# Kernel optimization log

Measured on AMD Instinct MI355X. Metric: run time of the kernel, lower is better.

The kernel has to match this reference:

```python
import jax, jax.numpy as jnp
import numpy as np

V, E, H, B, S, T = 32000, 256, 256, 64, 512, 256


def setup_inputs() -> dict:
    key = jax.random.key(0)
    ks = jax.random.split(key, 24)
    def w(i, shape, scale=0.05):
        return jax.random.normal(ks[i], shape, jnp.float32) * scale
    return {
        "pre_seq": jax.random.randint(ks[0], (B, S), 0, V),
        "post_seq": jax.random.randint(ks[1], (B, S), 0, V),
        "trg": jax.random.randint(ks[2], (B, T), 0, V),
        "emb": w(3, (V, E)),
        "Wi_pre": w(4, (3 * H, E)), "Wh_pre": w(5, (3 * H, H)),
        "bi_pre": w(6, (3 * H,)), "bh_pre": w(7, (3 * H,)),
        "Wi_post": w(8, (3 * H, E)), "Wh_post": w(9, (3 * H, H)),
        "bi_post": w(10, (3 * H,)), "bh_post": w(11, (3 * H,)),
        "Wfc": w(12, (H, 2 * H)), "bfc": w(13, (H,)),
        "Wi_dec": w(14, (3 * H, E)), "Wh_dec": w(15, (3 * H, H)),
        "bi_dec": w(16, (3 * H,)), "bh_dec": w(17, (3 * H,)),
        "w_hid": w(18, (1, 2 * H)), "b_hid": w(19, (1,)),
        "w_out": w(20, (1, 1)), "b_out": w(21, (1,)),
    }


def gru_cell(h, x, Wi, Wh, bi, bh):
    # torch nn.GRU gating convention, gates ordered (r, z, n)
    gi = x @ Wi.T + bi              # (B, 3H)
    gh = h @ Wh.T + bh              # (B, 3H)
    ir, iz, inn = jnp.split(gi, 3, axis=-1)
    hr, hz, hn = jnp.split(gh, 3, axis=-1)
    r = jax.nn.sigmoid(ir + hr)
    z = jax.nn.sigmoid(iz + hz)
    n = jnp.tanh(inn + r * hn)
    return (1.0 - z) * n + z * h


def gru_seq(seq_emb, Wi, Wh, bi, bh):
    # seq_emb: (B, L, E) -> outputs (B, L, H), final hidden (B, H)
    h0 = jnp.zeros((seq_emb.shape[0], Wh.shape[1]), seq_emb.dtype)
    def step(h, x):
        h = gru_cell(h, x, Wi, Wh, bi, bh)
        return h, h
    hT, outs = jax.lax.scan(step, h0, jnp.swapaxes(seq_emb, 0, 1))
    return jnp.swapaxes(outs, 0, 1), hT


def reference(pre_seq, post_seq, trg, emb, Wi_pre, Wh_pre, bi_pre, bh_pre,
              Wi_post, Wh_post, bi_post, bh_post, Wfc, bfc,
              Wi_dec, Wh_dec, bi_dec, bh_dec, w_hid, b_hid, w_out, b_out):
    # Encoder: two GRUs over pre/post token embeddings (dropout off / eval mode)
    pre_out, pre_h = gru_seq(emb[pre_seq], Wi_pre, Wh_pre, bi_pre, bh_pre)
    post_out, post_h = gru_seq(emb[post_seq], Wi_post, Wh_post, bi_post, bh_post)
    enc_out = jnp.concatenate([pre_out, post_out], axis=1)          # (B, 2S, H)
    h0 = jnp.tanh(jnp.concatenate([pre_h, post_h], axis=-1) @ Wfc.T + bfc)  # (B, H)

    # fc_hid(relu(cat([enc_out, h_t]))) splits into a step-constant enc term
    # and a per-step hidden term since relu acts elementwise on the concat.
    A = jax.nn.relu(enc_out) @ w_hid[0, :H]                         # (B, 2S)

    # Teacher-forced decoder inputs: last pre token, then trg[:, :-1]
    in_toks = jnp.concatenate([pre_seq[:, -1:], trg[:, :-1]], axis=1)  # (B, T)

    def step(h, tok):
        x = emb[tok]                                                # (B, E)
        h = gru_cell(h, x, Wi_dec, Wh_dec, bi_dec, bh_dec)          # (B, H)
        s = jax.nn.relu(h) @ w_hid[0, H:]                           # (B,)
        out = (A + s[:, None] + b_hid[0]) * w_out[0, 0] + b_out[0]  # (B, 2S)
        return h, out

    _, outs = jax.lax.scan(step, h0, in_toks.T)                     # (T, B, 2S)
    outs = jnp.swapaxes(outs, 0, 1)                                 # (B, T, 2S)
    return outs[:, :, :S], outs[:, :, S:]
```

## Files before the change

### kernel.cpp

```cpp
#include <hip/hip_runtime.h>
#include <stdint.h>

typedef _Float16 f16;
typedef _Float16 half2_t __attribute__((ext_vector_type(2)));
typedef _Float16 half8_t __attribute__((ext_vector_type(8)));
typedef float    f32x4_t __attribute__((ext_vector_type(4)));
typedef uint32_t u32x32  __attribute__((ext_vector_type(32)));

constexpr int NB = 64, NS = 512, NT = 256, NE = 256, NH = 256;
constexpr int G3 = 768;

static __device__ __forceinline__ float sigm(float x){ return 1.f/(1.f+__expf(-x)); }
static __device__ __forceinline__ float tanhfast(float x){
  float e = __expf(-2.f*x);
  return (1.f-e)/(1.f+e);
}
static __device__ __forceinline__ uint32_t pack2(float a, float b){
  half2_t h; h[0]=(f16)a; h[1]=(f16)b;
  return __builtin_bit_cast(uint32_t, h);
}
static __device__ __forceinline__ float dot2f(uint32_t w, uint32_t h, float acc){
#if __has_builtin(__builtin_amdgcn_fdot2)
  return __builtin_amdgcn_fdot2(__builtin_bit_cast(half2_t,w),
                                __builtin_bit_cast(half2_t,h), acc, false);
#else
  half2_t a = __builtin_bit_cast(half2_t,w), b = __builtin_bit_cast(half2_t,h);
  return acc + (float)a[0]*(float)b[0] + (float)a[1]*(float)b[1];
#endif
}
static __device__ __forceinline__ half8_t cvt8(float4 a, float4 b){
  half8_t p;
  p[0]=(f16)a.x; p[1]=(f16)a.y; p[2]=(f16)a.z; p[3]=(f16)a.w;
  p[4]=(f16)b.x; p[5]=(f16)b.y; p[6]=(f16)b.z; p[7]=(f16)b.w;
  return p;
}

#define LOAD_W(WSRC)                                                         \
  _Pragma("unroll")                                                          \
  for (int i=0;i<32;++i){                                                    \
    wr0[i]=(WSRC)[(size_t)i*G3];          wr1[i]=(WSRC)[(size_t)(i+32)*G3];  \
    wz0[i]=(WSRC)[(size_t)i*G3+256];      wz1[i]=(WSRC)[(size_t)(i+32)*G3+256];\
    wn0[i]=(WSRC)[(size_t)i*G3+512];      wn1[i]=(WSRC)[(size_t)(i+32)*G3+512];\
  }

#define DOT_BLOCK(W_R, W_Z, W_N, HPTR)                                       \
  _Pragma("unroll")                                                          \
  for (int c=0;c<4;++c){                                                     \
    uint4 ha = *(const uint4*)((HPTR) + c*8);                                \
    uint4 hb = *(const uint4*)((HPTR) + c*8 + 4);                            \
    uint32_t hh0=ha.x,hh1=ha.y,hh2=ha.z,hh3=ha.w;                            \
    uint32_t hh4=hb.x,hh5=hb.y,hh6=hb.z,hh7=hb.w;                            \
    a0=dot2f(W_R[c*8+0],hh0,a0); a1=dot2f(W_Z[c*8+0],hh0,a1); a2=dot2f(W_N[c*8+0],hh0,a2); \
    a0=dot2f(W_R[c*8+1],hh1,a0); a1=dot2f(W_Z[c*8+1],hh1,a1); a2=dot2f(W_N[c*8+1],hh1,a2); \
    a0=dot2f(W_R[c*8+2],hh2,a0); a1=dot2f(W_Z[c*8+2],hh2,a1); a2=dot2f(W_N[c*8+2],hh2,a2); \
    a0=dot2f(W_R[c*8+3],hh3,a0); a1=dot2f(W_Z[c*8+3],hh3,a1); a2=dot2f(W_N[c*8+3],hh3,a2); \
    a0=dot2f(W_R[c*8+4],hh4,a0); a1=dot2f(W_Z[c*8+4],hh4,a1); a2=dot2f(W_N[c*8+4],hh4,a2); \
    a0=dot2f(W_R[c*8+5],hh5,a0); a1=dot2f(W_Z[c*8+5],hh5,a1); a2=dot2f(W_N[c*8+5],hh5,a2); \
    a0=dot2f(W_R[c*8+6],hh6,a0); a1=dot2f(W_Z[c*8+6],hh6,a1); a2=dot2f(W_N[c*8+6],hh6,a2); \
    a0=dot2f(W_R[c*8+7],hh7,a0); a1=dot2f(W_Z[c*8+7],hh7,a1); a2=dot2f(W_N[c*8+7],hh7,a2); \
  }

__global__ __launch_bounds__(256) void k_prep(const float* __restrict__ Wh_pre,
                                              const float* __restrict__ Wh_post,
                                              const float* __restrict__ Wh_dec,
                                              uint32_t* __restrict__ WhT_pre,
                                              uint32_t* __restrict__ WhT_post,
                                              uint32_t* __restrict__ WhT_dec,
                                              const int* __restrict__ pre_seq,
                                              const int* __restrict__ trg,
                                              int* __restrict__ in_toks){
  int bid = blockIdx.x;
  if (bid < 1152){
    const float* Wh = (bid < 384) ? Wh_pre : (bid < 768) ? Wh_post : Wh_dec;
    uint32_t* out   = (bid < 384) ? WhT_pre : (bid < 768) ? WhT_post : WhT_dec;
    int idx = (bid % 384)*256 + threadIdx.x;
    int kp = idx / G3, row = idx % G3;
    out[idx] = pack2(Wh[(size_t)row*NE + 2*kp], Wh[(size_t)row*NE + 2*kp + 1]);
  } else {
    int idx = (bid - 1152)*256 + threadIdx.x;
    int b = idx >> 8, t = idx & 255;
    in_toks[idx] = (t == 0) ? pre_seq[b*NS + NS-1] : trg[b*NT + t - 1];
  }
}

__global__ __launch_bounds__(256) void k_gemm_gi(const float* __restrict__ emb,
                                                 const int* __restrict__ toks,
                                                 const float* __restrict__ Wi,
                                                 const float* __restrict__ bi,
                                                 f16* __restrict__ out){
  __shared__ f16 As[128][72];
  __shared__ f16 Bs[128][72];
  const int tid = threadIdx.x;
  const int m0 = blockIdx.x*128, n0 = blockIdx.y*128;
  const int lane = tid & 63, wid = tid >> 6;
  const int wm = wid >> 1, wn = wid & 1;
  const int fr = lane & 15, fq = lane >> 4;

  f32x4_t acc[4][4];
  #pragma unroll
  for (int i=0;i<4;++i)
    #pragma unroll
    for (int j=0;j<4;++j){ acc[i][j][0]=0.f; acc[i][j][1]=0.f; acc[i][j][2]=0.f; acc[i][j][3]=0.f; }

  const int r = tid >> 1, hh = tid & 1;
  const int tok = toks[m0 + r];
  const float* asrc = emb + (size_t)tok*NE + hh*32;
  const float* bsrc = Wi  + (size_t)(n0 + r)*NE + hh*32;

  for (int k0 = 0; k0 < NE; k0 += 64){
    #pragma unroll
    for (int c=0;c<4;++c){
      float4 x0 = *(const float4*)(asrc + k0 + c*8);
      float4 x1 = *(const float4*)(asrc + k0 + c*8 + 4);
      *(half8_t*)&As[r][hh*32 + c*8] = cvt8(x0, x1);
      float4 y0 = *(const float4*)(bsrc + k0 + c*8);
      float4 y1 = *(const float4*)(bsrc + k0 + c*8 + 4);
      *(half8_t*)&Bs[r][hh*32 + c*8] = cvt8(y0, y1);
    }
    __syncthreads();
    #pragma unroll
    for (int kk=0; kk<2; ++kk){
      half8_t af[4], bf[4];
      #pragma unroll
      for (int m=0;m<4;++m) af[m] = *(const half8_t*)&As[wm*64 + m*16 + fr][kk*32 + fq*8];
      #pragma unroll
      for (int n=0;n<4;++n) bf[n] = *(const half8_t*)&Bs[wn*64 + n*16 + fr][kk*32 + fq*8];
      #pragma unroll
      for (int m=0;m<4;++m)
        #pragma unroll
        for (int n=0;n<4;++n)
          acc[m][n] = __builtin_amdgcn_mfma_f32_16x16x32_f16(af[m], bf[n], acc[m][n], 0,0,0);
    }
    __syncthreads();
  }
  #pragma unroll
  for (int n=0;n<4;++n){
    const int col = n0 + wn*64 + n*16 + fr;
    const float bv = bi[col];
    #pragma unroll
    for (int m=0;m<4;++m){
      const int rowb = m0 + wm*64 + m*16 + fq*4;
      #pragma unroll
      for (int j=0;j<4;++j)
        out[(size_t)(rowb + j)*G3 + col] = (f16)(acc[m][n][j] + bv);
    }
  }
}

__global__ __launch_bounds__(512, 2) void k_enc(const uint32_t* __restrict__ WhT_pre,
                                                const uint32_t* __restrict__ WhT_post,
                                                const f16* __restrict__ gi_pre,
                                                const f16* __restrict__ gi_post,
                                                const float* __restrict__ bh_pre,
                                                const float* __restrict__ bh_post,
                                                const float* __restrict__ w_hid,
                                                float* __restrict__ Abuf,
                                                float* __restrict__ preh,
                                                float* __restrict__ posth){
  __shared__ __align__(16) uint32_t h_pair[128];
  __shared__ float part[3][256];
  __shared__ float ared[4];

  const int b = blockIdx.x & 63, which = blockIdx.x >> 6;
  const int tid = threadIdx.x;
  const int n = tid & 255, half = tid >> 8;

  const uint32_t* WhT = which ? WhT_post : WhT_pre;
  const f16* gi = (which ? gi_post : gi_pre) + (size_t)b*NS*G3;
  const float* bh = which ? bh_post : bh_pre;

  u32x32 wr0, wr1, wz0, wz1, wn0, wn1;
  {
    const uint32_t* wsrc = WhT + (size_t)(half*64)*G3 + n;
    LOAD_W(wsrc);
  }
  const float bh0 = bh[n], bh1 = bh[256+n], bh2 = bh[512+n];
  const float whv = w_hid[n];
  float hreg = 0.f;
  if (tid < 128) h_pair[tid] = 0u;
  __syncthreads();

  float* Arow = Abuf + b*1024 + which*512;

  for (int t=0; t<NS; ++t){
    float g0=0.f, g1=0.f, g2=0.f;
    if (half == 0){
      const f16* gp = gi + (size_t)t*G3;
      g0 = (float)gp[n]; g1 = (float)gp[256+n]; g2 = (float)gp[512+n];
    }
    float a0=0.f, a1=0.f, a2=0.f;
    const uint32_t* hp = h_pair + half*64;
    DOT_BLOCK(wr0, wz0, wn0, hp);
    DOT_BLOCK(wr1, wz1, wn1, hp + 32);
    if (half == 1){ part[0][n]=a0; part[1][n]=a1; part[2][n]=a2; }
    __syncthreads();
    if (half == 0){
      float ghr = a0 + part[0][n] + bh0;
      float ghz = a1 + part[1][n] + bh1;
      float ghn = a2 + part[2][n] + bh2;
      float rg = sigm(g0 + ghr);
      float zg = sigm(g1 + ghz);
      float nn = tanhfast(g2 + rg*ghn);
      float hnew = (1.f - zg)*nn + zg*hreg;
      hreg = hnew;
      float hnb = __shfl_down(hnew, 1);
      if ((n & 1) == 0) h_pair[n >> 1] = pack2(hnew, hnb);
      float redv = fmaxf(hnew, 0.f) * whv;
      #pragma unroll
      for (int off=32; off; off>>=1) redv += __shfl_down(redv, off);
      if ((tid & 63) == 0) ared[tid >> 6] = redv;
    }
    __syncthreads();
    if (tid == 0) Arow[t] = ared[0]+ared[1]+ared[2]+ared[3];
  }
  if (half == 0) (which ? posth : preh)[b*NH + n] = hreg;
}

__global__ __launch_bounds__(512, 2) void k_dec(const uint32_t* __restrict__ WhT,
                                                const f16* __restrict__ gi,
                                                const float* __restrict__ bh,
                                                const float* __restrict__ w_hid,
                                                const float* __restrict__ Wfc,
                                                const float* __restrict__ bfc,
                                                const float* __restrict__ preh,
                                                const float* __restrict__ posth,
                                                float* __restrict__ sbuf){
  __shared__ __align__(16) uint32_t h_pair[128];
  __shared__ float part[3][256];
  __shared__ float ared[4];
  __shared__ float hcat[512];

  const int b = blockIdx.x;
  const int tid = threadIdx.x;
  const int n = tid & 255, half = tid >> 8;

  const float bh0 = bh[n], bh1 = bh[256+n], bh2 = bh[512+n];
  const float whv = w_hid[NH + n];
  float hreg = 0.f;

  hcat[tid] = (tid < 256) ? preh[b*NH + tid] : posth[b*NH + tid - 256];
  __syncthreads();
  {
    const float* wrow = Wfc + (size_t)n*512 + half*256;
    const float* hc = hcat + half*256;
    float acc = 0.f;
    #pragma unroll 4
    for (int j=0;j<256;j+=4){
      float4 wv = *(const float4*)(wrow + j);
      acc = fmaf(wv.x, hc[j],   acc);
      acc = fmaf(wv.y, hc[j+1], acc);
      acc = fmaf(wv.z, hc[j+2], acc);
      acc = fmaf(wv.w, hc[j+3], acc);
    }
    if (half == 1) part[0][n] = acc;
    __syncthreads();
    if (half == 0){
      float h0 = tanhfast(acc + part[0][n] + bfc[n]);
      hreg = h0;
      float hnb = __shfl_down(h0, 1);
      if ((n & 1) == 0) h_pair[n >> 1] = pack2(h0, hnb);
    }
    __syncthreads();
  }

  u32x32 wr0, wr1, wz0, wz1, wn0, wn1;
  {
    const uint32_t* wsrc = WhT + (size_t)(half*64)*G3 + n;
    LOAD_W(wsrc);
  }

  const f16* gib = gi + (size_t)b*NT*G3;
  for (int t=0; t<NT; ++t){
    float g0=0.f, g1=0.f, g2=0.f;
    if (half == 0){
      const f16* gp = gib + (size_t)t*G3;
      g0 = (float)gp[n]; g1 = (float)gp[256+n]; g2 = (float)gp[512+n];
    }
    float a0=0.f, a1=0.f, a2=0.f;
    const uint32_t* hp = h_pair + half*64;
    DOT_BLOCK(wr0, wz0, wn0, hp);
    DOT_BLOCK(wr1, wz1, wn1, hp + 32);
    if (half == 1){ part[0][n]=a0; part[1][n]=a1; part[2][n]=a2; }
    __syncthreads();
    if (half == 0){
      float ghr = a0 + part[0][n] + bh0;
      float ghz = a1 + part[1][n] + bh1;
      float ghn = a2 + part[2][n] + bh2;
      float rg = sigm(g0 + ghr);
      float zg = sigm(g1 + ghz);
      float nn = tanhfast(g2 + rg*ghn);
      float hnew = (1.f - zg)*nn + zg*hreg;
      hreg = hnew;
      float hnb = __shfl_down(hnew, 1);
      if ((n & 1) == 0) h_pair[n >> 1] = pack2(hnew, hnb);
      float redv = fmaxf(hnew, 0.f) * whv;
      #pragma unroll
      for (int off=32; off; off>>=1) redv += __shfl_down(redv, off);
      if ((tid & 63) == 0) ared[tid >> 6] = redv;
    }
    __syncthreads();
    if (tid == 0) sbuf[b*NT + t] = ared[0]+ared[1]+ared[2]+ared[3];
  }
}

__global__ __launch_bounds__(256) void k_final(const float* __restrict__ Abuf,
                                               const float* __restrict__ sbuf,
                                               const float* __restrict__ b_hid,
                                               const float* __restrict__ w_out,
                                               const float* __restrict__ b_out,
                                               float* __restrict__ out){
  const float bh = b_hid[0], wo = w_out[0], bo = b_out[0];
  const int idx = blockIdx.x*256 + threadIdx.x;
  const int j4 = idx & 127, t = (idx >> 7) & 255, b = idx >> 15;
  const float sv = sbuf[b*NT + t] + bh;
  const float4 a0 = *(const float4*)(Abuf + b*1024 + j4*4);
  const float4 a1 = *(const float4*)(Abuf + b*1024 + 512 + j4*4);
  float4 o0, o1;
  o0.x = (a0.x + sv)*wo + bo; o0.y = (a0.y + sv)*wo + bo;
  o0.z = (a0.z + sv)*wo + bo; o0.w = (a0.w + sv)*wo + bo;
  o1.x = (a1.x + sv)*wo + bo; o1.y = (a1.y + sv)*wo + bo;
  o1.z = (a1.z + sv)*wo + bo; o1.w = (a1.w + sv)*wo + bo;
  float4* o = (float4*)out;
  o[idx] = o0;
  o[(size_t)(NB*NT*NS/4) + idx] = o1;
}

extern "C" void kernel_launch(void* const* d_in, const int* in_sizes, int n_in,
                              void* d_out, int out_size, void* d_ws, size_t ws_size,
                              hipStream_t stream){
  const int*   pre_seq = (const int*)d_in[0];
  const int*   post_seq= (const int*)d_in[1];
  const int*   trg     = (const int*)d_in[2];
  const float* emb     = (const float*)d_in[3];
  const float* Wi_pre  = (const float*)d_in[4];
  const float* Wh_pre  = (const float*)d_in[5];
  const float* bi_pre  = (const float*)d_in[6];
  const float* bh_pre  = (const float*)d_in[7];
  const float* Wi_post = (const float*)d_in[8];
  const float* Wh_post = (const float*)d_in[9];
  const float* bi_post = (const float*)d_in[10];
  const float* bh_post = (const float*)d_in[11];
  const float* Wfc     = (const float*)d_in[12];
  const float* bfc     = (const float*)d_in[13];
  const float* Wi_dec  = (const float*)d_in[14];
  const float* Wh_dec  = (const float*)d_in[15];
  const float* bi_dec  = (const float*)d_in[16];
  const float* bh_dec  = (const float*)d_in[17];
  const float* w_hid   = (const float*)d_in[18];
  const float* b_hid   = (const float*)d_in[19];
  const float* w_out   = (const float*)d_in[20];
  const float* b_out   = (const float*)d_in[21];

  char* wp = (char*)d_ws;
  f16* gi_pre  = (f16*)wp; wp += (size_t)NB*NS*G3*2;
  f16* gi_post = (f16*)wp; wp += (size_t)NB*NS*G3*2;
  f16* gi_dec  = (f16*)wp; wp += (size_t)NB*NT*G3*2;
  uint32_t* WhT_pre  = (uint32_t*)wp; wp += (size_t)128*G3*4;
  uint32_t* WhT_post = (uint32_t*)wp; wp += (size_t)128*G3*4;
  uint32_t* WhT_dec  = (uint32_t*)wp; wp += (size_t)128*G3*4;
  int*   in_toks = (int*)wp;   wp += (size_t)NB*NT*4;
  float* Abuf    = (float*)wp; wp += (size_t)NB*1024*4;
  float* sbuf    = (float*)wp; wp += (size_t)NB*NT*4;
  float* preh    = (float*)wp; wp += (size_t)NB*NH*4;
  float* posth   = (float*)wp; wp += (size_t)NB*NH*4;
  (void)ws_size; (void)in_sizes; (void)n_in; (void)out_size;

  k_prep<<<1216, 256, 0, stream>>>(Wh_pre, Wh_post, Wh_dec,
                                   WhT_pre, WhT_post, WhT_dec,
                                   pre_seq, trg, in_toks);

  k_gemm_gi<<<dim3(256,6), 256, 0, stream>>>(emb, pre_seq,  Wi_pre,  bi_pre,  gi_pre);
  k_gemm_gi<<<dim3(256,6), 256, 0, stream>>>(emb, post_seq, Wi_post, bi_post, gi_post);
  k_gemm_gi<<<dim3(128,6), 256, 0, stream>>>(emb, in_toks,  Wi_dec,  bi_dec,  gi_dec);

  k_enc<<<128, 512, 0, stream>>>(WhT_pre, WhT_post, gi_pre, gi_post,
                                 bh_pre, bh_post, w_hid, Abuf, preh, posth);
  k_dec<<<64, 512, 0, stream>>>(WhT_dec, gi_dec, bh_dec, w_hid, Wfc, bfc,
                                preh, posth, sbuf);
  k_final<<<NB*NT*NS/4/256, 256, 0, stream>>>(Abuf, sbuf, b_hid, w_out, b_out,
                                              (float*)d_out);
}
```

Before: 1.280 ms.

## Split GRU recurrent matvec across four thread quarters with redundant gate math

The encoder and decoder recurrent kernels move from 512 to 1024 threads per block, so each thread holds a quarter of the K dimension (96 weight registers instead of 192) pinned with asm barriers. All four quarters exchange partial sums through shared memory and compute the gate nonlinearities redundantly, so no thread sits idle after the barrier. The hidden state is now stored as plain f16 rather than packed pairs via shuffle. The reduction result for each step is written lazily at the start of the next step, which drops one barrier per step. The aim is to shorten the per-step serial critical path. The cost is more shared-memory traffic and 1024-thread blocks with one block per CU.

Result: slower. 1.417 ms (+10.7%).

```diff
diff --git a/kernel.cpp b/kernel.cpp
--- a/kernel.cpp
+++ b/kernel.cpp
@@ -5,7 +5,7 @@
 typedef _Float16 half2_t __attribute__((ext_vector_type(2)));
 typedef _Float16 half8_t __attribute__((ext_vector_type(8)));
 typedef float    f32x4_t __attribute__((ext_vector_type(4)));
-typedef uint32_t u32x32  __attribute__((ext_vector_type(32)));
+typedef uint32_t u32x4   __attribute__((ext_vector_type(4)));
 
 constexpr int NB = 64, NS = 512, NT = 256, NE = 256, NH = 256;
 constexpr int G3 = 768;
@@ -35,30 +35,29 @@
   return p;
 }
 
-#define LOAD_W(WSRC)                                                         \
-  _Pragma("unroll")                                                          \
-  for (int i=0;i<32;++i){                                                    \
-    wr0[i]=(WSRC)[(size_t)i*G3];          wr1[i]=(WSRC)[(size_t)(i+32)*G3];  \
-    wz0[i]=(WSRC)[(size_t)i*G3+256];      wz1[i]=(WSRC)[(size_t)(i+32)*G3+256];\
-    wn0[i]=(WSRC)[(size_t)i*G3+512];      wn1[i]=(WSRC)[(size_t)(i+32)*G3+512];\
-  }
-
-#define DOT_BLOCK(W_R, W_Z, W_N, HPTR)                                       \
-  _Pragma("unroll")                                                          \
-  for (int c=0;c<4;++c){                                                     \
-    uint4 ha = *(const uint4*)((HPTR) + c*8);                                \
-    uint4 hb = *(const uint4*)((HPTR) + c*8 + 4);                            \
-    uint32_t hh0=ha.x,hh1=ha.y,hh2=ha.z,hh3=ha.w;                            \
-    uint32_t hh4=hb.x,hh5=hb.y,hh6=hb.z,hh7=hb.w;                            \
-    a0=dot2f(W_R[c*8+0],hh0,a0); a1=dot2f(W_Z[c*8+0],hh0,a1); a2=dot2f(W_N[c*8+0],hh0,a2); \
-    a0=dot2f(W_R[c*8+1],hh1,a0); a1=dot2f(W_Z[c*8+1],hh1,a1); a2=dot2f(W_N[c*8+1],hh1,a2); \
-    a0=dot2f(W_R[c*8+2],hh2,a0); a1=dot2f(W_Z[c*8+2],hh2,a1); a2=dot2f(W_N[c*8+2],hh2,a2); \
-    a0=dot2f(W_R[c*8+3],hh3,a0); a1=dot2f(W_Z[c*8+3],hh3,a1); a2=dot2f(W_N[c*8+3],hh3,a2); \
-    a0=dot2f(W_R[c*8+4],hh4,a0); a1=dot2f(W_Z[c*8+4],hh4,a1); a2=dot2f(W_N[c*8+4],hh4,a2); \
-    a0=dot2f(W_R[c*8+5],hh5,a0); a1=dot2f(W_Z[c*8+5],hh5,a1); a2=dot2f(W_N[c*8+5],hh5,a2); \
-    a0=dot2f(W_R[c*8+6],hh6,a0); a1=dot2f(W_Z[c*8+6],hh6,a1); a2=dot2f(W_N[c*8+6],hh6,a2); \
-    a0=dot2f(W_R[c*8+7],hh7,a0); a1=dot2f(W_Z[c*8+7],hh7,a1); a2=dot2f(W_N[c*8+7],hh7,a2); \
-  }
+#define DECLW(P, GO, C)                                                      \
+  uint32_t P##C##_0 = wsrc[(size_t)((C)*4+0)*G3 + (GO)];                     \
+  uint32_t P##C##_1 = wsrc[(size_t)((C)*4+1)*G3 + (GO)];                     \
+  uint32_t P##C##_2 = wsrc[(size_t)((C)*4+2)*G3 + (GO)];                     \
+  uint32_t P##C##_3 = wsrc[(size_t)((C)*4+3)*G3 + (GO)];                     \
+  asm volatile("" : "+v"(P##C##_0), "+v"(P##C##_1), "+v"(P##C##_2), "+v"(P##C##_3));
+
+#define DECL_ALL_W \
+  DECLW(wa,0,0) DECLW(wa,0,1) DECLW(wa,0,2) DECLW(wa,0,3)                    \
+  DECLW(wa,0,4) DECLW(wa,0,5) DECLW(wa,0,6) DECLW(wa,0,7)                    \
+  DECLW(wb,256,0) DECLW(wb,256,1) DECLW(wb,256,2) DECLW(wb,256,3)            \
+  DECLW(wb,256,4) DECLW(wb,256,5) DECLW(wb,256,6) DECLW(wb,256,7)            \
+  DECLW(wc,512,0) DECLW(wc,512,1) DECLW(wc,512,2) DECLW(wc,512,3)            \
+  DECLW(wc,512,4) DECLW(wc,512,5) DECLW(wc,512,6) DECLW(wc,512,7)
+
+#define DOTC(C) {                                                            \
+    u32x4 hq = *(const u32x4*)(h32q + 4*(C));                                \
+    a0=dot2f(wa##C##_0,hq[0],a0); a1=dot2f(wb##C##_0,hq[0],a1); a2=dot2f(wc##C##_0,hq[0],a2); \
+    a0=dot2f(wa##C##_1,hq[1],a0); a1=dot2f(wb##C##_1,hq[1],a1); a2=dot2f(wc##C##_1,hq[1],a2); \
+    a0=dot2f(wa##C##_2,hq[2],a0); a1=dot2f(wb##C##_2,hq[2],a1); a2=dot2f(wc##C##_2,hq[2],a2); \
+    a0=dot2f(wa##C##_3,hq[3],a0); a1=dot2f(wb##C##_3,hq[3],a1); a2=dot2f(wc##C##_3,hq[3],a2); }
+
+#define DOT_ALL DOTC(0) DOTC(1) DOTC(2) DOTC(3) DOTC(4) DOTC(5) DOTC(6) DOTC(7)
 
 __global__ __launch_bounds__(256) void k_prep(const float* __restrict__ Wh_pre,
                                               const float* __restrict__ Wh_post,
@@ -147,160 +146,162 @@
   }
 }
 
-__global__ __launch_bounds__(512, 2) void k_enc(const uint32_t* __restrict__ WhT_pre,
-                                                const uint32_t* __restrict__ WhT_post,
-                                                const f16* __restrict__ gi_pre,
-                                                const f16* __restrict__ gi_post,
-                                                const float* __restrict__ bh_pre,
-                                                const float* __restrict__ bh_post,
-                                                const float* __restrict__ w_hid,
-                                                float* __restrict__ Abuf,
-                                                float* __restrict__ preh,
-                                                float* __restrict__ posth){
-  __shared__ __align__(16) uint32_t h_pair[128];
-  __shared__ float part[3][256];
+__global__ __launch_bounds__(1024) void k_enc(const uint32_t* __restrict__ WhT_pre,
+                                              const uint32_t* __restrict__ WhT_post,
+                                              const f16* __restrict__ gi_pre,
+                                              const f16* __restrict__ gi_post,
+                                              const float* __restrict__ bh_pre,
+                                              const float* __restrict__ bh_post,
+                                              const float* __restrict__ w_hid,
+                                              float* __restrict__ Abuf,
+                                              float* __restrict__ preh,
+                                              float* __restrict__ posth){
+  __shared__ __align__(16) f16 hh16[256];
+  __shared__ __align__(16) float part[4][256][4];
   __shared__ float ared[4];
 
   const int b = blockIdx.x & 63, which = blockIdx.x >> 6;
   const int tid = threadIdx.x;
-  const int n = tid & 255, half = tid >> 8;
+  const int n = tid & 255, q = tid >> 8;
 
   const uint32_t* WhT = which ? WhT_post : WhT_pre;
-  const f16* gi = (which ? gi_post : gi_pre) + (size_t)b*NS*G3;
   const float* bh = which ? bh_post : bh_pre;
 
-  u32x32 wr0, wr1, wz0, wz1, wn0, wn1;
-  {
-    const uint32_t* wsrc = WhT + (size_t)(half*64)*G3 + n;
-    LOAD_W(wsrc);
-  }
+  const uint32_t* wsrc = WhT + (size_t)(q*32)*G3 + n;
+  DECL_ALL_W
+
   const float bh0 = bh[n], bh1 = bh[256+n], bh2 = bh[512+n];
   const float whv = w_hid[n];
   float hreg = 0.f;
-  if (tid < 128) h_pair[tid] = 0u;
+  if (tid < 128) ((uint32_t*)hh16)[tid] = 0u;
   __syncthreads();
 
   float* Arow = Abuf + b*1024 + which*512;
-
+  const uint32_t* h32q = (const uint32_t*)hh16 + q*32;
+  const f16* gp = (which ? gi_post : gi_pre) + (size_t)b*NS*G3 + n;
+
+  #pragma unroll 1
   for (int t=0; t<NS; ++t){
-    float g0=0.f, g1=0.f, g2=0.f;
-    if (half == 0){
-      const f16* gp = gi + (size_t)t*G3;
-      g0 = (float)gp[n]; g1 = (float)gp[256+n]; g2 = (float)gp[512+n];
-    }
+    if (tid == 768 && t > 0) Arow[t-1] = ared[0]+ared[1]+ared[2]+ared[3];
+    f16 gr16 = gp[0], gz16 = gp[256], gn16 = gp[512];
+    gp += G3;
     float a0=0.f, a1=0.f, a2=0.f;
-    const uint32_t* hp = h_pair + half*64;
-    DOT_BLOCK(wr0, wz0, wn0, hp);
-    DOT_BLOCK(wr1, wz1, wn1, hp + 32);
-    if (half == 1){ part[0][n]=a0; part[1][n]=a1; part[2][n]=a2; }
-    __syncthreads();
-    if (half == 0){
-      float ghr = a0 + part[0][n] + bh0;
-      float ghz = a1 + part[1][n] + bh1;
-      float ghn = a2 + part[2][n] + bh2;
-      float rg = sigm(g0 + ghr);
-      float zg = sigm(g1 + ghz);
-      float nn = tanhfast(g2 + rg*ghn);
-      float hnew = (1.f - zg)*nn + zg*hreg;
-      hreg = hnew;
-      float hnb = __shfl_down(hnew, 1);
-      if ((n & 1) == 0) h_pair[n >> 1] = pack2(hnew, hnb);
+    DOT_ALL
+    *(f32x4_t*)&part[q][n][0] = (f32x4_t){a0, a1, a2, 0.f};
+    __syncthreads();
+    float s0=a0, s1=a1, s2=a2;
+    {
+      f32x4_t p1 = *(const f32x4_t*)&part[(q+1)&3][n][0];
+      s0+=p1[0]; s1+=p1[1]; s2+=p1[2];
+      f32x4_t p2 = *(const f32x4_t*)&part[(q+2)&3][n][0];
+      s0+=p2[0]; s1+=p2[1]; s2+=p2[2];
+      f32x4_t p3 = *(const f32x4_t*)&part[(q+3)&3][n][0];
+      s0+=p3[0]; s1+=p3[1]; s2+=p3[2];
+    }
+    float rg = sigm((float)gr16 + s0 + bh0);
+    float zg = sigm((float)gz16 + s1 + bh1);
+    float nn = tanhfast((float)gn16 + rg*(s2 + bh2));
+    float hnew = (1.f - zg)*nn + zg*hreg;
+    hreg = hnew;
+    if (q == 0) hh16[n] = (f16)hnew;
+    if (q == 1){
       float redv = fmaxf(hnew, 0.f) * whv;
       #pragma unroll
       for (int off=32; off; off>>=1) redv += __shfl_down(redv, off);
-      if ((tid & 63) == 0) ared[tid >> 6] = redv;
-    }
-    __syncthreads();
-    if (tid == 0) Arow[t] = ared[0]+ared[1]+ared[2]+ared[3];
-  }
-  if (half == 0) (which ? posth : preh)[b*NH + n] = hreg;
-}
-
-__global__ __launch_bounds__(512, 2) void k_dec(const uint32_t* __restrict__ WhT,
-                                                const f16* __restrict__ gi,
-                                                const float* __restrict__ bh,
-                                                const float* __restrict__ w_hid,
-                                                const float* __restrict__ Wfc,
-                                                const float* __restrict__ bfc,
-                                                const float* __restrict__ preh,
-                                                const float* __restrict__ posth,
-                                                float* __restrict__ sbuf){
-  __shared__ __align__(16) uint32_t h_pair[128];
-  __shared__ float part[3][256];
+      if ((tid & 63) == 0) ared[(tid >> 6) & 3] = redv;
+    }
+    __syncthreads();
+  }
+  if (tid == 768) Arow[NS-1] = ared[0]+ared[1]+ared[2]+ared[3];
+  if (q == 0) (which ? posth : preh)[b*NH + n] = hreg;
+}
+
+__global__ __launch_bounds__(1024) void k_dec(const uint32_t* __restrict__ WhT,
+                                              const f16* __restrict__ gi,
+                                              const float* __restrict__ bh,
+                                              const float* __restrict__ w_hid,
+                                              const float* __restrict__ Wfc,
+                                              const float* __restrict__ bfc,
+                                              const float* __restrict__ preh,
+                                              const float* __restrict__ posth,
+                                              float* __restrict__ sbuf){
+  __shared__ __align__(16) f16 hh16[256];
+  __shared__ __align__(16) float part[4][256][4];
   __shared__ float ared[4];
   __shared__ float hcat[512];
 
   const int b = blockIdx.x;
   const int tid = threadIdx.x;
-  const int n = tid & 255, half = tid >> 8;
+  const int n = tid & 255, q = tid >> 8;
+
+  const uint32_t* wsrc = WhT + (size_t)(q*32)*G3 + n;
+  DECL_ALL_W
 
   const float bh0 = bh[n], bh1 = bh[256+n], bh2 = bh[512+n];
   const float whv = w_hid[NH + n];
-  float hreg = 0.f;
-
-  hcat[tid] = (tid < 256) ? preh[b*NH + tid] : posth[b*NH + tid - 256];
+  float hreg;
+
+  if (tid < 256) hcat[tid] = preh[b*NH + tid];
+  else if (tid < 512) hcat[tid] = posth[b*NH + tid - 256];
   __syncthreads();
   {
-    const float* wrow = Wfc + (size_t)n*512 + half*256;
-    const float* hc = hcat + half*256;
+    const float* wrow = Wfc + (size_t)n*512 + q*128;
+    const float* hc = hcat + q*128;
     float acc = 0.f;
     #pragma unroll 4
-    for (int j=0;j<256;j+=4){
+    for (int j=0;j<128;j+=4){
       float4 wv = *(const float4*)(wrow + j);
       acc = fmaf(wv.x, hc[j],   acc);
       acc = fmaf(wv.y, hc[j+1], acc);
       acc = fmaf(wv.z, hc[j+2], acc);
       acc = fmaf(wv.w, hc[j+3], acc);
     }
-    if (half == 1) part[0][n] = acc;
-    __syncthreads();
-    if (half == 0){
-      float h0 = tanhfast(acc + part[0][n] + bfc[n]);
-      hreg = h0;
-      float hnb = __shfl_down(h0, 1);
-      if ((n & 1) == 0) h_pair[n >> 1] = pack2(h0, hnb);
-    }
-    __syncthreads();
-  }
-
-  u32x32 wr0, wr1, wz0, wz1, wn0, wn1;
-  {
-    const uint32_t* wsrc = WhT + (size_t)(half*64)*G3 + n;
-    LOAD_W(wsrc);
-  }
-
-  const f16* gib = gi + (size_t)b*NT*G3;
+    part[q][n][0] = acc;
+    __syncthreads();
+    float s = part[0][n][0] + part[1][n][0] + part[2][n][0] + part[3][n][0];
+    float h0 = tanhfast(s + bfc[n]);
+    hreg = h0;
+    if (q == 0) hh16[n] = (f16)h0;
+    __syncthreads();
+  }
+
+  float* srow = sbuf + b*NT;
+  const uint32_t* h32q = (const uint32_t*)hh16 + q*32;
+  const f16* gp = gi + (size_t)b*NT*G3 + n;
+
+  #pragma unroll 1
   for (int t=0; t<NT; ++t){
-    float g0=0.f, g1=0.f, g2=0.f;
-    if (half == 0){
-      const f16* gp = gib + (size_t)t*G3;
-      g0 = (float)gp[n]; g1 = (float)gp[256+n]; g2 = (float)gp[512+n];
-    }
+    if (tid == 768 && t > 0) srow[t-1] = ared[0]+ared[1]+ared[2]+ared[3];
+    f16 gr16 = gp[0], gz16 = gp[256], gn16 = gp[512];
+    gp += G3;
     float a0=0.f, a1=0.f, a2=0.f;
-    const uint32_t* hp = h_pair + half*64;
-    DOT_BLOCK(wr0, wz0, wn0, hp);
-    DOT_BLOCK(wr1, wz1, wn1, hp + 32);
-    if (half == 1){ part[0][n]=a0; part[1][n]=a1; part[2][n]=a2; }
-    __syncthreads();
-    if (half == 0){
-      float ghr = a0 + part[0][n] + bh0;
-      float ghz = a1 + part[1][n] + bh1;
-      float ghn = a2 + part[2][n] + bh2;
-      float rg = sigm(g0 + ghr);
-      float zg = sigm(g1 + ghz);
-      float nn = tanhfast(g2 + rg*ghn);
-      float hnew = (1.f - zg)*nn + zg*hreg;
-      hreg = hnew;
-      float hnb = __shfl_down(hnew, 1);
-      if ((n & 1) == 0) h_pair[n >> 1] = pack2(hnew, hnb);
+    DOT_ALL
+    *(f32x4_t*)&part[q][n][0] = (f32x4_t){a0, a1, a2, 0.f};
+    __syncthreads();
+    float s0=a0, s1=a1, s2=a2;
+    {
+      f32x4_t p1 = *(const f32x4_t*)&part[(q+1)&3][n][0];
+      s0+=p1[0]; s1+=p1[1]; s2+=p1[2];
+      f32x4_t p2 = *(const f32x4_t*)&part[(q+2)&3][n][0];
+      s0+=p2[0]; s1+=p2[1]; s2+=p2[2];
+      f32x4_t p3 = *(const f32x4_t*)&part[(q+3)&3][n][0];
+      s0+=p3[0]; s1+=p3[1]; s2+=p3[2];
+    }
+    float rg = sigm((float)gr16 + s0 + bh0);
+    float zg = sigm((float)gz16 + s1 + bh1);
+    float nn = tanhfast((float)gn16 + rg*(s2 + bh2));
+    float hnew = (1.f - zg)*nn + zg*hreg;
+    hreg = hnew;
+    if (q == 0) hh16[n] = (f16)hnew;
+    if (q == 1){
       float redv = fmaxf(hnew, 0.f) * whv;
       #pragma unroll
       for (int off=32; off; off>>=1) redv += __shfl_down(redv, off);
-      if ((tid & 63) == 0) ared[tid >> 6] = redv;
-    }
-    __syncthreads();
-    if (tid == 0) sbuf[b*NT + t] = ared[0]+ared[1]+ared[2]+ared[3];
-  }
+      if ((tid & 63) == 0) ared[(tid >> 6) & 3] = redv;
+    }
+    __syncthreads();
+  }
+  if (tid == 768) srow[NT-1] = ared[0]+ared[1]+ared[2]+ared[3];
 }
 
 __global__ __launch_bounds__(256) void k_final(const float* __restrict__ Abuf,
@@ -373,10 +374,10 @@
   k_gemm_gi<<<dim3(256,6), 256, 0, stream>>>(emb, post_seq, Wi_post, bi_post, gi_post);
   k_gemm_gi<<<dim3(128,6), 256, 0, stream>>>(emb, in_toks,  Wi_dec,  bi_dec,  gi_dec);
 
-  k_enc<<<128, 512, 0, stream>>>(WhT_pre, WhT_post, gi_pre, gi_post,
-                                 bh_pre, bh_post, w_hid, Abuf, preh, posth);
-  k_dec<<<64, 512, 0, stream>>>(WhT_dec, gi_dec, bh_dec, w_hid, Wfc, bfc,
-                                preh, posth, sbuf);
+  k_enc<<<128, 1024, 0, stream>>>(WhT_pre, WhT_post, gi_pre, gi_post,
+                                  bh_pre, bh_post, w_hid, Abuf, preh, posth);
+  k_dec<<<64, 1024, 0, stream>>>(WhT_dec, gi_dec, bh_dec, w_hid, Wfc, bfc,
+                                 preh, posth, sbuf);
   k_final<<<NB*NT*NS/4/256, 256, 0, stream>>>(Abuf, sbuf, b_hid, w_out, b_out,
                                               (float*)d_out);
 }
```

## Split recurrent weights between registers and per-step streamed global loads

Applied to the files above, without the earlier changes.

Each thread now keeps only half of its recurrent weight slice in registers (the first 32 k-pairs per gate) and streams the other half from a newly prepacked, coalesced global layout every timestep with inline global_load_dwordx4 and manual vmcnt waits. The loads are interleaved with the register-resident dot products so memory latency overlaps compute. The goal is to cut register pressure, which was holding 192 weight registers per thread, possibly to avoid spills or allow better scheduling. The cost is repeated L2 traffic for the weights on every step of a latency-bound serial recurrence, plus a larger prep kernel.

Measured after the change: 1.973 ms. +54.2%, slower.

```diff
diff --git a/kernel.cpp b/kernel.cpp
--- a/kernel.cpp
+++ b/kernel.cpp
@@ -5,7 +5,7 @@
 typedef _Float16 half2_t __attribute__((ext_vector_type(2)));
 typedef _Float16 half8_t __attribute__((ext_vector_type(8)));
 typedef float    f32x4_t __attribute__((ext_vector_type(4)));
-typedef uint32_t u32x32  __attribute__((ext_vector_type(32)));
+typedef uint32_t u32x4   __attribute__((ext_vector_type(4)));
 
 constexpr int NB = 64, NS = 512, NT = 256, NE = 256, NH = 256;
 constexpr int G3 = 768;
@@ -35,30 +35,61 @@
   return p;
 }
 
-#define LOAD_W(WSRC)                                                         \
-  _Pragma("unroll")                                                          \
-  for (int i=0;i<32;++i){                                                    \
-    wr0[i]=(WSRC)[(size_t)i*G3];          wr1[i]=(WSRC)[(size_t)(i+32)*G3];  \
-    wz0[i]=(WSRC)[(size_t)i*G3+256];      wz1[i]=(WSRC)[(size_t)(i+32)*G3+256];\
-    wn0[i]=(WSRC)[(size_t)i*G3+512];      wn1[i]=(WSRC)[(size_t)(i+32)*G3+512];\
-  }
-
-#define DOT_BLOCK(W_R, W_Z, W_N, HPTR)                                       \
-  _Pragma("unroll")                                                          \
-  for (int c=0;c<4;++c){                                                     \
-    uint4 ha = *(const uint4*)((HPTR) + c*8);                                \
-    uint4 hb = *(const uint4*)((HPTR) + c*8 + 4);                            \
-    uint32_t hh0=ha.x,hh1=ha.y,hh2=ha.z,hh3=ha.w;                            \
-    uint32_t hh4=hb.x,hh5=hb.y,hh6=hb.z,hh7=hb.w;                            \
-    a0=dot2f(W_R[c*8+0],hh0,a0); a1=dot2f(W_Z[c*8+0],hh0,a1); a2=dot2f(W_N[c*8+0],hh0,a2); \
-    a0=dot2f(W_R[c*8+1],hh1,a0); a1=dot2f(W_Z[c*8+1],hh1,a1); a2=dot2f(W_N[c*8+1],hh1,a2); \
-    a0=dot2f(W_R[c*8+2],hh2,a0); a1=dot2f(W_Z[c*8+2],hh2,a1); a2=dot2f(W_N[c*8+2],hh2,a2); \
-    a0=dot2f(W_R[c*8+3],hh3,a0); a1=dot2f(W_Z[c*8+3],hh3,a1); a2=dot2f(W_N[c*8+3],hh3,a2); \
-    a0=dot2f(W_R[c*8+4],hh4,a0); a1=dot2f(W_Z[c*8+4],hh4,a1); a2=dot2f(W_N[c*8+4],hh4,a2); \
-    a0=dot2f(W_R[c*8+5],hh5,a0); a1=dot2f(W_Z[c*8+5],hh5,a1); a2=dot2f(W_N[c*8+5],hh5,a2); \
-    a0=dot2f(W_R[c*8+6],hh6,a0); a1=dot2f(W_Z[c*8+6],hh6,a1); a2=dot2f(W_N[c*8+6],hh6,a2); \
-    a0=dot2f(W_R[c*8+7],hh7,a0); a1=dot2f(W_Z[c*8+7],hh7,a1); a2=dot2f(W_N[c*8+7],hh7,a2); \
-  }
+#define PDECL(g, C)                                                          \
+  u32x4 p##g##_##C = { wsrc[(size_t)((C)*4+0)*G3 + (g)*256],                 \
+                       wsrc[(size_t)((C)*4+1)*G3 + (g)*256],                 \
+                       wsrc[(size_t)((C)*4+2)*G3 + (g)*256],                 \
+                       wsrc[(size_t)((C)*4+3)*G3 + (g)*256] };               \
+  asm volatile("" : "+v"(p##g##_##C));
+#define PDECL_G(g) PDECL(g,0) PDECL(g,1) PDECL(g,2) PDECL(g,3)               \
+                   PDECL(g,4) PDECL(g,5) PDECL(g,6) PDECL(g,7)
+#define PDECL_ALL PDECL_G(0) PDECL_G(1) PDECL_G(2)
+
+#define PDOT1(g, C, ACC) {                                                   \
+    u32x4 hq = *(const u32x4*)(hp + 4*(C));                                  \
+    ACC = dot2f(p##g##_##C[0], hq[0], ACC);                                  \
+    ACC = dot2f(p##g##_##C[1], hq[1], ACC);                                  \
+    ACC = dot2f(p##g##_##C[2], hq[2], ACC);                                  \
+    ACC = dot2f(p##g##_##C[3], hq[3], ACC); }
+#define PDOT_G(g, ACC) PDOT1(g,0,ACC) PDOT1(g,1,ACC) PDOT1(g,2,ACC)          \
+                       PDOT1(g,3,ACC) PDOT1(g,4,ACC) PDOT1(g,5,ACC)          \
+                       PDOT1(g,6,ACC) PDOT1(g,7,ACC)
+
+#define SISSUE1(g, cc)                                                       \
+  u32x4 s##g##_##cc;                                                         \
+  asm volatile("global_load_dwordx4 %0, %1, %2"                             \
+               : "=v"(s##g##_##cc)                                           \
+               : "v"(vbase + (uint32_t)(((g)*8+(cc))*4096)), "s"(WhS));
+#define SISSUE(g) SISSUE1(g,0) SISSUE1(g,1) SISSUE1(g,2) SISSUE1(g,3)        \
+                  SISSUE1(g,4) SISSUE1(g,5) SISSUE1(g,6) SISSUE1(g,7)
+
+#define SDOT1(g, cc, ACC) {                                                  \
+    u32x4 hq = *(const u32x4*)(hp + 32 + 4*(cc));                            \
+    ACC = dot2f(s##g##_##cc[0], hq[0], ACC);                                 \
+    ACC = dot2f(s##g##_##cc[1], hq[1], ACC);                                 \
+    ACC = dot2f(s##g##_##cc[2], hq[2], ACC);                                 \
+    ACC = dot2f(s##g##_##cc[3], hq[3], ACC); }
+#define SDOT_G(g, ACC) SDOT1(g,0,ACC) SDOT1(g,1,ACC) SDOT1(g,2,ACC)          \
+                       SDOT1(g,3,ACC) SDOT1(g,4,ACC) SDOT1(g,5,ACC)          \
+                       SDOT1(g,6,ACC) SDOT1(g,7,ACC)
+
+#define VMWAIT(N) do { asm volatile("s_waitcnt vmcnt(" #N ")");              \
+  __builtin_amdgcn_sched_barrier(0); } while(0)
+
+#define STEP_DOTS                                                            \
+    float a0=0.f, a1=0.f, a2=0.f;                                            \
+    SISSUE(0)                                                                \
+    PDOT_G(0, a0)                                                            \
+    SISSUE(1)                                                                \
+    VMWAIT(8);                                                               \
+    SDOT_G(0, a0)                                                            \
+    PDOT_G(1, a1)                                                            \
+    SISSUE(2)                                                                \
+    VMWAIT(8);                                                               \
+    SDOT_G(1, a1)                                                            \
+    PDOT_G(2, a2)                                                            \
+    VMWAIT(0);                                                               \
+    SDOT_G(2, a2)
 
 __global__ __launch_bounds__(256) void k_prep(const float* __restrict__ Wh_pre,
                                               const float* __restrict__ Wh_post,
@@ -66,6 +97,9 @@
                                               uint32_t* __restrict__ WhT_pre,
                                               uint32_t* __restrict__ WhT_post,
                                               uint32_t* __restrict__ WhT_dec,
+                                              uint32_t* __restrict__ WhS_pre,
+                                              uint32_t* __restrict__ WhS_post,
+                                              uint32_t* __restrict__ WhS_dec,
                                               const int* __restrict__ pre_seq,
                                               const int* __restrict__ trg,
                                               int* __restrict__ in_toks){
@@ -76,10 +110,22 @@
     int idx = (bid % 384)*256 + threadIdx.x;
     int kp = idx / G3, row = idx % G3;
     out[idx] = pack2(Wh[(size_t)row*NE + 2*kp], Wh[(size_t)row*NE + 2*kp + 1]);
-  } else {
+  } else if (bid < 1216){
     int idx = (bid - 1152)*256 + threadIdx.x;
     int b = idx >> 8, t = idx & 255;
     in_toks[idx] = (t == 0) ? pre_seq[b*NS + NS-1] : trg[b*NT + t - 1];
+  } else {
+    int bid2 = bid - 1216;
+    const float* Wh = (bid2 < 192) ? Wh_pre : (bid2 < 384) ? Wh_post : Wh_dec;
+    uint32_t* out   = (bid2 < 192) ? WhS_pre : (bid2 < 384) ? WhS_post : WhS_dec;
+    int j = (bid2 % 192)*256 + threadIdx.x;
+    int quad = j >> 2, e = j & 3;
+    int n = quad & 255, r = quad >> 8;
+    int half = r / 24, rr = r % 24;
+    int g = rr >> 3, cc = rr & 7;
+    int kp = half*64 + 32 + cc*4 + e;
+    out[j] = pack2(Wh[(size_t)(g*256 + n)*NE + 2*kp],
+                   Wh[(size_t)(g*256 + n)*NE + 2*kp + 1]);
   }
 }
 
@@ -147,16 +193,19 @@
   }
 }
 
-__global__ __launch_bounds__(512, 2) void k_enc(const uint32_t* __restrict__ WhT_pre,
-                                                const uint32_t* __restrict__ WhT_post,
-                                                const f16* __restrict__ gi_pre,
-                                                const f16* __restrict__ gi_post,
-                                                const float* __restrict__ bh_pre,
-                                                const float* __restrict__ bh_post,
-                                                const float* __restrict__ w_hid,
-                                                float* __restrict__ Abuf,
-                                                float* __restrict__ preh,
-                                                float* __restrict__ posth){
+__attribute__((amdgpu_flat_work_group_size(512,512), amdgpu_waves_per_eu(2,2)))
+__global__ void k_enc(const uint32_t* __restrict__ WhT_pre,
+                      const uint32_t* __restrict__ WhT_post,
+                      const uint32_t* __restrict__ WhS_pre,
+                      const uint32_t* __restrict__ WhS_post,
+                      const f16* __restrict__ gi_pre,
+                      const f16* __restrict__ gi_post,
+                      const float* __restrict__ bh_pre,
+                      const float* __restrict__ bh_post,
+                      const float* __restrict__ w_hid,
+                      float* __restrict__ Abuf,
+                      float* __restrict__ preh,
+                      float* __restrict__ posth){
   __shared__ __align__(16) uint32_t h_pair[128];
   __shared__ float part[3][256];
   __shared__ float ared[4];
@@ -166,14 +215,14 @@
   const int n = tid & 255, half = tid >> 8;
 
   const uint32_t* WhT = which ? WhT_post : WhT_pre;
+  const uint32_t* WhS = which ? WhS_post : WhS_pre;
   const f16* gi = (which ? gi_post : gi_pre) + (size_t)b*NS*G3;
   const float* bh = which ? bh_post : bh_pre;
 
-  u32x32 wr0, wr1, wz0, wz1, wn0, wn1;
-  {
-    const uint32_t* wsrc = WhT + (size_t)(half*64)*G3 + n;
-    LOAD_W(wsrc);
-  }
+  const uint32_t* wsrc = WhT + (size_t)(half*64)*G3 + n;
+  PDECL_ALL
+  const uint32_t vbase = (uint32_t)(half*98304 + n*16);
+
   const float bh0 = bh[n], bh1 = bh[256+n], bh2 = bh[512+n];
   const float whv = w_hid[n];
   float hreg = 0.f;
@@ -181,17 +230,17 @@
   __syncthreads();
 
   float* Arow = Abuf + b*1024 + which*512;
-
+  const uint32_t* hp = h_pair + half*64;
+  const f16* gp = gi + n;
+
+  #pragma unroll 1
   for (int t=0; t<NS; ++t){
     float g0=0.f, g1=0.f, g2=0.f;
     if (half == 0){
-      const f16* gp = gi + (size_t)t*G3;
-      g0 = (float)gp[n]; g1 = (float)gp[256+n]; g2 = (float)gp[512+n];
-    }
-    float a0=0.f, a1=0.f, a2=0.f;
-    const uint32_t* hp = h_pair + half*64;
-    DOT_BLOCK(wr0, wz0, wn0, hp);
-    DOT_BLOCK(wr1, wz1, wn1, hp + 32);
+      g0 = (float)gp[0]; g1 = (float)gp[256]; g2 = (float)gp[512];
+    }
+    gp += G3;
+    STEP_DOTS
     if (half == 1){ part[0][n]=a0; part[1][n]=a1; part[2][n]=a2; }
     __syncthreads();
     if (half == 0){
@@ -216,15 +265,17 @@
   if (half == 0) (which ? posth : preh)[b*NH + n] = hreg;
 }
 
-__global__ __launch_bounds__(512, 2) void k_dec(const uint32_t* __restrict__ WhT,
-                                                const f16* __restrict__ gi,
-                                                const float* __restrict__ bh,
-                                                const float* __restrict__ w_hid,
-                                                const float* __restrict__ Wfc,
-                                                const float* __restrict__ bfc,
-                                                const float* __restrict__ preh,
-                                                const float* __restrict__ posth,
-                                                float* __restrict__ sbuf){
+__attribute__((amdgpu_flat_work_group_size(512,512), amdgpu_waves_per_eu(2,2)))
+__global__ void k_dec(const uint32_t* __restrict__ WhT,
+                      const uint32_t* __restrict__ WhS,
+                      const f16* __restrict__ gi,
+                      const float* __restrict__ bh,
+                      const float* __restrict__ w_hid,
+                      const float* __restrict__ Wfc,
+                      const float* __restrict__ bfc,
+                      const float* __restrict__ preh,
+                      const float* __restrict__ posth,
+                      float* __restrict__ sbuf){
   __shared__ __align__(16) uint32_t h_pair[128];
   __shared__ float part[3][256];
   __shared__ float ared[4];
@@ -233,6 +284,10 @@
   const int b = blockIdx.x;
   const int tid = threadIdx.x;
   const int n = tid & 255, half = tid >> 8;
+
+  const uint32_t* wsrc = WhT + (size_t)(half*64)*G3 + n;
+  PDECL_ALL
+  const uint32_t vbase = (uint32_t)(half*98304 + n*16);
 
   const float bh0 = bh[n], bh1 = bh[256+n], bh2 = bh[512+n];
   const float whv = w_hid[NH + n];
@@ -263,23 +318,18 @@
     __syncthreads();
   }
 
-  u32x32 wr0, wr1, wz0, wz1, wn0, wn1;
-  {
-    const uint32_t* wsrc = WhT + (size_t)(half*64)*G3 + n;
-    LOAD_W(wsrc);
-  }
-
-  const f16* gib = gi + (size_t)b*NT*G3;
+  float* srow = sbuf + b*NT;
+  const uint32_t* hp = h_pair + half*64;
+  const f16* gp = gi + (size_t)b*NT*G3 + n;
+
+  #pragma unroll 1
   for (int t=0; t<NT; ++t){
     float g0=0.f, g1=0.f, g2=0.f;
     if (half == 0){
-      const f16* gp = gib + (size_t)t*G3;
-      g0 = (float)gp[n]; g1 = (float)gp[256+n]; g2 = (float)gp[512+n];
-    }
-    float a0=0.f, a1=0.f, a2=0.f;
-    const uint32_t* hp = h_pair + half*64;
-    DOT_BLOCK(wr0, wz0, wn0, hp);
-    DOT_BLOCK(wr1, wz1, wn1, hp + 32);
+      g0 = (float)gp[0]; g1 = (float)gp[256]; g2 = (float)gp[512];
+    }
+    gp += G3;
+    STEP_DOTS
     if (half == 1){ part[0][n]=a0; part[1][n]=a1; part[2][n]=a2; }
     __syncthreads();
     if (half == 0){
@@ -299,7 +349,7 @@
       if ((tid & 63) == 0) ared[tid >> 6] = redv;
     }
     __syncthreads();
-    if (tid == 0) sbuf[b*NT + t] = ared[0]+ared[1]+ared[2]+ared[3];
+    if (tid == 0) srow[t] = ared[0]+ared[1]+ared[2]+ared[3];
   }
 }
 
@@ -358,6 +408,9 @@
   uint32_t* WhT_pre  = (uint32_t*)wp; wp += (size_t)128*G3*4;
   uint32_t* WhT_post = (uint32_t*)wp; wp += (size_t)128*G3*4;
   uint32_t* WhT_dec  = (uint32_t*)wp; wp += (size_t)128*G3*4;
+  uint32_t* WhS_pre  = (uint32_t*)wp; wp += (size_t)49152*4;
+  uint32_t* WhS_post = (uint32_t*)wp; wp += (size_t)49152*4;
+  uint32_t* WhS_dec  = (uint32_t*)wp; wp += (size_t)49152*4;
   int*   in_toks = (int*)wp;   wp += (size_t)NB*NT*4;
   float* Abuf    = (float*)wp; wp += (size_t)NB*1024*4;
   float* sbuf    = (float*)wp; wp += (size_t)NB*NT*4;
@@ -365,17 +418,19 @@
   float* posth   = (float*)wp; wp += (size_t)NB*NH*4;
   (void)ws_size; (void)in_sizes; (void)n_in; (void)out_size;
 
-  k_prep<<<1216, 256, 0, stream>>>(Wh_pre, Wh_post, Wh_dec,
+  k_prep<<<1792, 256, 0, stream>>>(Wh_pre, Wh_post, Wh_dec,
                                    WhT_pre, WhT_post, WhT_dec,
+                                   WhS_pre, WhS_post, WhS_dec,
                                    pre_seq, trg, in_toks);
 
   k_gemm_gi<<<dim3(256,6), 256, 0, stream>>>(emb, pre_seq,  Wi_pre,  bi_pre,  gi_pre);
   k_gemm_gi<<<dim3(256,6), 256, 0, stream>>>(emb, post_seq, Wi_post, bi_post, gi_post);
   k_gemm_gi<<<dim3(128,6), 256, 0, stream>>>(emb, in_toks,  Wi_dec,  bi_dec,  gi_dec);
 
-  k_enc<<<128, 512, 0, stream>>>(WhT_pre, WhT_post, gi_pre, gi_post,
-                                 bh_pre, bh_post, w_hid, Abuf, preh, posth);
-  k_dec<<<64, 512, 0, stream>>>(WhT_dec, gi_dec, bh_dec, w_hid, Wfc, bfc,
+  k_enc<<<128, 512, 0, stream>>>(WhT_pre, WhT_post, WhS_pre, WhS_post,
+                                 gi_pre, gi_post, bh_pre, bh_post, w_hid,
+                                 Abuf, preh, posth);
+  k_dec<<<64, 512, 0, stream>>>(WhT_dec, WhS_dec, gi_dec, bh_dec, w_hid, Wfc, bfc,
                                 preh, posth, sbuf);
   k_final<<<NB*NT*NS/4/256, 256, 0, stream>>>(Abuf, sbuf, b_hid, w_out, b_out,
                                               (float*)d_out);
```
